# Kernel optimization log

Measured on AMD Instinct MI355X. Metric: run time of the kernel, lower is better.

Reference implementation:

```python
import jax, jax.numpy as jnp
import numpy as np

ATTRACTION_W = 1.0
REPULSION_W = 1.0
MARGIN = 0.3  # hardcoded local `margin = 0.3` in the torch forward


def setup_inputs() -> dict:
    key = jax.random.key(0)
    k1, k2, k3 = jax.random.split(key, 3)
    B, N, D, K = 16, 65536, 32, 512
    beta = jax.random.normal(k1, (B, N, 1), dtype=jnp.float32)
    embed = jax.random.normal(k2, (B, N, D), dtype=jnp.float32)
    # instance id per hit: -1 = background, 0..K-1 = instances
    sid = jax.random.randint(k3, (B, N), -1, K).astype(jnp.int32)
    # first K hits are the condensation points, one per instance
    sid = sid.at[:, :K].set(jnp.arange(K, dtype=jnp.int32)[None, :])
    is_cp = jnp.zeros((B, N), dtype=jnp.int32).at[:, :K].set(1)
    return {"beta": beta, "embed": embed, "slice_id": sid, "is_cp": is_cp, "num_instances": K}


def _per_batch(beta_b, emb_b, sid, iscp, K):
    # beta_b: [N], emb_b: [N, D], sid/iscp: [N]
    N = sid.shape[0]
    cp = iscp == 1
    valid = sid >= 0
    noncp = valid & ~cp  # non-cp signal hits
    pos = cp.sum().astype(jnp.float32)
    neg = jnp.float32(N) - pos  # noncp + background
    pos_w = jax.lax.stop_gradient(neg / (pos + 1e-6))
    w = jnp.where(cp, pos_w, jnp.where(noncp, 1.0, 2.0))
    # weighted BCE-with-logits, reduction='mean'
    x = beta_b
    y = cp.astype(jnp.float32)
    bce = jnp.maximum(x, 0.0) - x * y + jnp.log1p(jnp.exp(-jnp.abs(x)))
    beta_ce = (w * bce).mean()

    # segment id: valid hits -> sid, background -> dummy segment K (dropped)
    seg = jnp.where(valid, sid, K)
    counts = jax.ops.segment_sum(valid.astype(jnp.float32), seg, num_segments=K + 1)[:K]
    inst_exists = counts > 0  # the `unique()` set

    # first cp hit index per instance (sentinel N if instance has no cp)
    idxs = jnp.arange(N)
    first_cp = jax.ops.segment_min(jnp.where(cp & valid, idxs, N), seg, num_segments=K + 1)[:K]
    has_cp = first_cp < N
    safe_cp = jnp.minimum(first_cp, N - 1)
    cp_emb = emb_b[safe_cp]  # [K, D]
    cp_beta = beta_b[safe_cp]  # [K]

    # attraction: sum over instances (with a cp) of mean ||e_hit - e_cp||^2
    sid_c = jnp.clip(sid, 0, K - 1)
    d2 = ((emb_b - cp_emb[sid_c]) ** 2).sum(-1)  # [N]
    d2 = jnp.where(valid, d2, 0.0)
    seg_d2 = jax.ops.segment_sum(d2, seg, num_segments=K + 1)[:K]
    attr = (jnp.where(has_cp & inst_exists, seg_d2 / jnp.maximum(counts, 1.0), 0.0).sum()
            * ATTRACTION_W)

    # ranking: instances with exactly 1 cp and >0 noncp hits
    cp_count = jax.ops.segment_sum((cp & valid).astype(jnp.float32), seg, num_segments=K + 1)[:K]
    ncp_count = jax.ops.segment_sum(noncp.astype(jnp.float32), seg, num_segments=K + 1)[:K]
    r = jax.nn.relu(beta_b + MARGIN - cp_beta[sid_c])
    r = jnp.where(noncp, r, 0.0)
    seg_r = jax.ops.segment_sum(r, seg, num_segments=K + 1)[:K]
    qual = (cp_count == 1.0) & (ncp_count > 0)
    n_unique = inst_exists.sum().astype(jnp.float32)
    ranking = (jnp.where(qual, seg_r / jnp.maximum(ncp_count, 1.0), 0.0).sum()
               / jnp.maximum(n_unique, 1.0))

    beta_loss = beta_ce + 2.0 * ranking

    # repulsion over all cp hits; data has exactly one cp per instance so the
    # cp set equals cp_emb (K points), matching torch's emb_b[cp_idx]
    diff = cp_emb[:, None, :] - cp_emb[None, :, :]  # [K, K, D]
    rep = jnp.exp(-(diff ** 2).sum(-1)).mean() * REPULSION_W

    return beta_loss + attr + rep, beta_loss, attr, rep


def reference(beta, embed, slice_id, is_cp, num_instances):
    K = int(num_instances)
    beta2 = beta[..., 0]  # squeeze(-1)
    loss_b, bl, al, rl = jax.vmap(lambda b, e, s, c: _per_batch(b, e, s, c, K))(
        beta2, embed, slice_id, is_cp)
    return loss_b.mean(), bl.mean(), al.mean(), rl.mean()
```

## Files before the change

### kernel.cpp

```cpp
#include <hip/hip_runtime.h>
#include <math.h>

#define N_HITS 65536
#define K_INST 512
#define MARGIN 0.3f
#define BPB    128
#define HITS_PB (N_HITS / BPB)

__global__ __launch_bounds__(256) void k_scan(
    const int* __restrict__ sid, const int* __restrict__ iscp,
    int* first_cp, int* pos_cnt) {
    int b = blockIdx.y;
    size_t bo = (size_t)b * N_HITS;
    int i = blockIdx.x * 256 + threadIdx.x;
    int stride = gridDim.x * 256;
    for (; i < N_HITS; i += stride) {
        int c = iscp[bo + i];
        if (c == 1) {
            atomicAdd(&pos_cnt[b], 1);
            int s = sid[bo + i];
            if (s >= 0) atomicMin(&first_cp[b * K_INST + s], i);
        }
    }
}

__global__ __launch_bounds__(256) void k_gather(
    const float* __restrict__ beta, const float4* __restrict__ embed4,
    const int* __restrict__ first_cp,
    float* cp_beta, float4* cp_emb4, int B) {
    int g = blockIdx.x * 256 + threadIdx.x;
    int total = B * K_INST * 8;
    if (g >= total) return;
    int row = g >> 3, sub = g & 7;
    int b = row / K_INST;
    int fc = first_cp[row];
    int safe = min(fc, N_HITS - 1);
    cp_emb4[(size_t)row * 8 + sub] = embed4[((size_t)b * N_HITS + safe) * 8 + sub];
    if (sub == 0) cp_beta[row] = beta[b * N_HITS + safe];
}

__global__ __launch_bounds__(256) void k_main(
    const float*  __restrict__ beta,  const float4* __restrict__ embed4,
    const int*    __restrict__ sid_g, const int*    __restrict__ iscp_g,
    const float4* __restrict__ cp_emb4, const float* __restrict__ cp_beta,
    int* cnt_packed, float* seg_d2, float* seg_r,
    float* s_cp, float* s_ncp, float* s_bg) {
    __shared__ int   l_cnt[K_INST];
    __shared__ float l_d2[K_INST];
    __shared__ float l_r[K_INST];
    __shared__ float l_cb[K_INST];
    __shared__ float l_red[12];

    int b = blockIdx.y, tid = threadIdx.x;
    size_t bo = (size_t)b * N_HITS;
    int base = blockIdx.x * HITS_PB;

    for (int k = tid; k < K_INST; k += 256) {
        l_cnt[k] = 0; l_d2[k] = 0.f; l_r[k] = 0.f;
        l_cb[k] = cp_beta[b * K_INST + k];
    }
    __syncthreads();

    const float4* cpe = cp_emb4 + (size_t)b * K_INST * 8;
    float a_cp = 0.f, a_ncp = 0.f, a_bg = 0.f;

#pragma unroll
    for (int h = 0; h < HITS_PB / 256; ++h) {
        int i = base + h * 256 + tid;
        int s = sid_g[bo + i];
        int c = iscp_g[bo + i];
        float x = beta[bo + i];
        int sc = min(max(s, 0), K_INST - 1);
        const float4* ep  = embed4 + (bo + i) * 8;
        const float4* cpp = cpe + (size_t)sc * 8;

        float d2 = 0.f;
#pragma unroll
        for (int j = 0; j < 8; ++j) {
            float4 e = ep[j], ce = cpp[j];
            float dx = e.x - ce.x, dy = e.y - ce.y;
            float dz = e.z - ce.z, dw = e.w - ce.w;
            d2 += dx * dx + dy * dy + dz * dz + dw * dw;
        }

        bool cp = (c == 1), valid = (s >= 0), noncp = valid && !cp;
        float t = __expf(-fabsf(x));
        float bce = fmaxf(x, 0.f) - (cp ? x : 0.f) + __logf(1.f + t);
        if (cp) a_cp += bce; else if (noncp) a_ncp += bce; else a_bg += bce;
        if (valid) {
            atomicAdd(&l_cnt[s], cp ? (1 << 20) : 1);
            atomicAdd(&l_d2[s], d2);
            if (noncp) {
                float r = fmaxf(x + MARGIN - l_cb[s], 0.f);
                atomicAdd(&l_r[s], r);
            }
        }
    }

    for (int o = 32; o > 0; o >>= 1) {
        a_cp  += __shfl_down(a_cp, o);
        a_ncp += __shfl_down(a_ncp, o);
        a_bg  += __shfl_down(a_bg, o);
    }
    int wave = tid >> 6;
    if ((tid & 63) == 0) { l_red[wave] = a_cp; l_red[4 + wave] = a_ncp; l_red[8 + wave] = a_bg; }
    __syncthreads();
    if (tid == 0) {
        atomicAdd(&s_cp[b],  l_red[0] + l_red[1] + l_red[2]  + l_red[3]);
        atomicAdd(&s_ncp[b], l_red[4] + l_red[5] + l_red[6]  + l_red[7]);
        atomicAdd(&s_bg[b],  l_red[8] + l_red[9] + l_red[10] + l_red[11]);
    }
    for (int k = tid; k < K_INST; k += 256) {
        int   cv = l_cnt[k]; if (cv)        atomicAdd(&cnt_packed[b * K_INST + k], cv);
        float dv = l_d2[k];  if (dv != 0.f) atomicAdd(&seg_d2[b * K_INST + k], dv);
        float rv = l_r[k];   if (rv != 0.f) atomicAdd(&seg_r[b * K_INST + k], rv);
    }
}

__global__ __launch_bounds__(512) void k_tail(
    const float4* __restrict__ cp_emb4,
    const int* __restrict__ cnt_packed, const float* __restrict__ seg_d2,
    const float* __restrict__ seg_r, const int* __restrict__ first_cp,
    const int* __restrict__ pos_cnt, const float* __restrict__ s_cp,
    const float* __restrict__ s_ncp, const float* __restrict__ s_bg,
    float* attr_b, float* rank_b, float* nuniq_b, float* rep_b,
    int* ctr, float* out, int B) {
    int tid = threadIdx.x;
    int nrep = B * 16;

    if ((int)blockIdx.x < nrep) {
        __shared__ float4 tile[32 * 8];
        __shared__ float red[8];
        int b = blockIdx.x >> 4, t2 = blockIdx.x & 15;
        const float4* base = cp_emb4 + (size_t)b * K_INST * 8;
        float4 r0[8];
#pragma unroll
        for (int cc = 0; cc < 8; ++cc) r0[cc] = base[(size_t)tid * 8 + cc];
        if (tid < 256) tile[tid] = base[(size_t)t2 * 256 + tid];
        __syncthreads();
        float acc = 0.f;
        for (int j = 0; j < 32; ++j) {
            float d2 = 0.f;
#pragma unroll
            for (int cc = 0; cc < 8; ++cc) {
                float4 ev = tile[j * 8 + cc];
                float ax = r0[cc].x - ev.x, ay = r0[cc].y - ev.y;
                float az = r0[cc].z - ev.z, aw = r0[cc].w - ev.w;
                d2 += ax * ax + ay * ay + az * az + aw * aw;
            }
            acc += __expf(-d2);
        }
        for (int o = 32; o > 0; o >>= 1) acc += __shfl_down(acc, o);
        if ((tid & 63) == 0) red[tid >> 6] = acc;
        __syncthreads();
        if (tid == 0) {
            float t = 0.f;
            for (int w = 0; w < 8; ++w) t += red[w];
            atomicAdd(&rep_b[b], t);
        }
    } else {
        __shared__ float red2[3][8];
        int b = blockIdx.x - nrep, k = tid;
        int v = cnt_packed[b * K_INST + k];
        int ncp = v & 0xFFFFF, cpc = v >> 20;
        int counts = ncp + cpc;
        int fc = first_cp[b * K_INST + k];
        bool has_cp = fc < N_HITS, exists = counts > 0;
        float attr = (has_cp && exists) ? seg_d2[b * K_INST + k] / fmaxf((float)counts, 1.f) : 0.f;
        float rank = (cpc == 1 && ncp > 0) ? seg_r[b * K_INST + k] / fmaxf((float)ncp, 1.f) : 0.f;
        float uq = exists ? 1.f : 0.f;
        for (int o = 32; o > 0; o >>= 1) {
            attr += __shfl_down(attr, o);
            rank += __shfl_down(rank, o);
            uq   += __shfl_down(uq, o);
        }
        if ((k & 63) == 0) { red2[0][k >> 6] = attr; red2[1][k >> 6] = rank; red2[2][k >> 6] = uq; }
        __syncthreads();
        if (k == 0) {
            float a = 0.f, r = 0.f, u = 0.f;
            for (int w = 0; w < 8; ++w) { a += red2[0][w]; r += red2[1][w]; u += red2[2][w]; }
            attr_b[b] = a; rank_b[b] = r; nuniq_b[b] = u;
        }
    }

    __shared__ int is_last;
    __syncthreads();
    if (tid == 0) {
        __threadfence();
        int v = atomicAdd(ctr, 1);
        is_last = (v == (int)gridDim.x - 1);
    }
    __syncthreads();
    if (is_last) {
        __threadfence();
        if (tid < 64) {
            int b = tid;
            float loss = 0.f, bl = 0.f, at = 0.f, rp = 0.f;
            if (b < B) {
                float pos = (float)pos_cnt[b];
                float pw = ((float)N_HITS - pos) / (pos + 1e-6f);
                float bce = (pw * s_cp[b] + s_ncp[b] + 2.f * s_bg[b]) / (float)N_HITS;
                float rank = rank_b[b] / fmaxf(nuniq_b[b], 1.f);
                bl = bce + 2.f * rank;
                at = attr_b[b];
                rp = rep_b[b] / (float)(K_INST * K_INST);
                loss = bl + at + rp;
            }
            for (int o = 32; o > 0; o >>= 1) {
                loss += __shfl_down(loss, o);
                bl   += __shfl_down(bl, o);
                at   += __shfl_down(at, o);
                rp   += __shfl_down(rp, o);
            }
            if (tid == 0) {
                float inv = 1.f / (float)B;
                out[0] = loss * inv;
                out[1] = bl * inv;
                out[2] = at * inv;
                out[3] = rp * inv;
            }
        }
    }
}

extern "C" void kernel_launch(void* const* d_in, const int* in_sizes, int n_in,
                              void* d_out, int out_size, void* d_ws, size_t ws_size,
                              hipStream_t stream) {
    const float*  beta   = (const float*)d_in[0];
    const float*  embed  = (const float*)d_in[1];
    const int*    sid    = (const int*)d_in[2];
    const int*    iscp   = (const int*)d_in[3];
    float* out = (float*)d_out;

    int BN = in_sizes[0];
    int B  = BN / N_HITS;
    int BK = B * K_INST;

    char* ws = (char*)d_ws;
    int*   cnt_packed = (int*)ws;
    float* seg_d2     = (float*)(ws + 4 * (size_t)BK);
    float* seg_r      = (float*)(ws + 8 * (size_t)BK);
    float* scal       = (float*)(ws + 12 * (size_t)BK);
    int*   pos_cnt  = (int*)scal;
    float* s_cp     = scal + 1 * B;
    float* s_ncp    = scal + 2 * B;
    float* s_bg     = scal + 3 * B;
    float* attr_b   = scal + 4 * B;
    float* rank_b   = scal + 5 * B;
    float* nuniq_b  = scal + 6 * B;
    float* rep_b    = scal + 7 * B;
    int*   ctr      = (int*)(scal + 8 * B);
    size_t zbytes = 12 * (size_t)BK + 32 * (size_t)B + 16;
    int*    first_cp = (int*)(ws + zbytes);
    float*  cp_beta  = (float*)(ws + zbytes + 4 * (size_t)BK);
    float4* cp_emb4  = (float4*)(ws + zbytes + 8 * (size_t)BK);

    hipMemsetAsync(ws, 0, zbytes, stream);
    hipMemsetAsync(first_cp, 0x7F, 4 * (size_t)BK, stream);

    k_scan<<<dim3(32, B), 256, 0, stream>>>(sid, iscp, first_cp, pos_cnt);

    k_gather<<<(BK * 8 + 255) / 256, 256, 0, stream>>>(beta, (const float4*)embed,
                                                       first_cp, cp_beta, cp_emb4, B);

    k_main<<<dim3(BPB, B), 256, 0, stream>>>(beta, (const float4*)embed, sid, iscp,
                                             (const float4*)cp_emb4, cp_beta,
                                             cnt_packed, seg_d2, seg_r, s_cp, s_ncp, s_bg);

    k_tail<<<B * 16 + B, 512, 0, stream>>>(cp_emb4, cnt_packed, seg_d2, seg_r,
                                           first_cp, pos_cnt, s_cp, s_ncp, s_bg,
                                           attr_b, rank_b, nuniq_b, rep_b,
                                           ctr, out, B);
}
```

Before: 261.7 us.

## Stage bf16 condensation-point embeddings in LDS and expand distance algebraically

The gather kernel now also writes a bf16, XOR-swizzled copy of the per-instance condensation-point embeddings. k_main loads that copy into shared memory and computes the distance in a second pass in which 8 lanes share each hit with coalesced float4 loads. It accumulates e·(e−2c) per instance into 4-way split shared bins, and the tail adds count·||c||² back. This removes scattered global reads of cp embeddings and the serial per-thread 32-float loop. In exchange, sid is read twice, there are more LDS atomics, and bf16 cp values plus the expanded form can cost precision through cancellation.

```diff
diff --git a/kernel.cpp b/kernel.cpp
--- a/kernel.cpp
+++ b/kernel.cpp
@@ -6,6 +6,14 @@
 #define MARGIN 0.3f
 #define BPB    128
 #define HITS_PB (N_HITS / BPB)
+
+__device__ __forceinline__ unsigned short f2bf(float f) {
+    unsigned u = __float_as_uint(f);
+    return (unsigned short)((u + 0x7FFFu + ((u >> 16) & 1u)) >> 16);
+}
+__device__ __forceinline__ float bf2f(unsigned short h) {
+    return __uint_as_float(((unsigned)h) << 16);
+}
 
 __global__ __launch_bounds__(256) void k_scan(
     const int* __restrict__ sid, const int* __restrict__ iscp,
@@ -27,7 +35,7 @@
 __global__ __launch_bounds__(256) void k_gather(
     const float* __restrict__ beta, const float4* __restrict__ embed4,
     const int* __restrict__ first_cp,
-    float* cp_beta, float4* cp_emb4, int B) {
+    float* cp_beta, float4* cp_emb4, ushort4* cpb_g, int B) {
     int g = blockIdx.x * 256 + threadIdx.x;
     int total = B * K_INST * 8;
     if (g >= total) return;
@@ -35,65 +43,76 @@
     int b = row / K_INST;
     int fc = first_cp[row];
     int safe = min(fc, N_HITS - 1);
-    cp_emb4[(size_t)row * 8 + sub] = embed4[((size_t)b * N_HITS + safe) * 8 + sub];
+    float4 e = embed4[((size_t)b * N_HITS + safe) * 8 + sub];
+    cp_emb4[(size_t)row * 8 + sub] = e;
+    ushort4 h;
+    h.x = f2bf(e.x); h.y = f2bf(e.y); h.z = f2bf(e.z); h.w = f2bf(e.w);
+    cpb_g[(size_t)row * 8 + (sub ^ (row & 7))] = h;
     if (sub == 0) cp_beta[row] = beta[b * N_HITS + safe];
 }
 
 __global__ __launch_bounds__(256) void k_main(
-    const float*  __restrict__ beta,  const float4* __restrict__ embed4,
-    const int*    __restrict__ sid_g, const int*    __restrict__ iscp_g,
-    const float4* __restrict__ cp_emb4, const float* __restrict__ cp_beta,
+    const float*  __restrict__ beta,
+    const float4* __restrict__ embed4,
+    const int*    __restrict__ sid_g, const int* __restrict__ iscp_g,
+    const ushort4* __restrict__ cpb_g, const float* __restrict__ cp_beta,
     int* cnt_packed, float* seg_d2, float* seg_r,
     float* s_cp, float* s_ncp, float* s_bg) {
-    __shared__ int   l_cnt[K_INST];
-    __shared__ float l_d2[K_INST];
-    __shared__ float l_r[K_INST];
-    __shared__ float l_cb[K_INST];
-    __shared__ float l_red[12];
+    __shared__ ushort4 cpb[K_INST * 8];
+    __shared__ float   d2p[K_INST * 4];
+    __shared__ int     l_cnt[K_INST];
+    __shared__ float   l_r[K_INST];
+    __shared__ float   l_cb[K_INST];
+    __shared__ float   l_red[12];
 
     int b = blockIdx.y, tid = threadIdx.x;
     size_t bo = (size_t)b * N_HITS;
     int base = blockIdx.x * HITS_PB;
 
     for (int k = tid; k < K_INST; k += 256) {
-        l_cnt[k] = 0; l_d2[k] = 0.f; l_r[k] = 0.f;
+        l_cnt[k] = 0; l_r[k] = 0.f;
         l_cb[k] = cp_beta[b * K_INST + k];
     }
+    for (int k = tid; k < K_INST * 4; k += 256) d2p[k] = 0.f;
+    {
+        const ushort4* src = cpb_g + (size_t)b * K_INST * 8;
+        for (int k = tid; k < K_INST * 8; k += 256) cpb[k] = src[k];
+    }
     __syncthreads();
 
-    const float4* cpe = cp_emb4 + (size_t)b * K_INST * 8;
     float a_cp = 0.f, a_ncp = 0.f, a_bg = 0.f;
-
 #pragma unroll
     for (int h = 0; h < HITS_PB / 256; ++h) {
         int i = base + h * 256 + tid;
         int s = sid_g[bo + i];
         int c = iscp_g[bo + i];
         float x = beta[bo + i];
-        int sc = min(max(s, 0), K_INST - 1);
-        const float4* ep  = embed4 + (bo + i) * 8;
-        const float4* cpp = cpe + (size_t)sc * 8;
-
-        float d2 = 0.f;
-#pragma unroll
-        for (int j = 0; j < 8; ++j) {
-            float4 e = ep[j], ce = cpp[j];
-            float dx = e.x - ce.x, dy = e.y - ce.y;
-            float dz = e.z - ce.z, dw = e.w - ce.w;
-            d2 += dx * dx + dy * dy + dz * dz + dw * dw;
-        }
-
         bool cp = (c == 1), valid = (s >= 0), noncp = valid && !cp;
         float t = __expf(-fabsf(x));
         float bce = fmaxf(x, 0.f) - (cp ? x : 0.f) + __logf(1.f + t);
         if (cp) a_cp += bce; else if (noncp) a_ncp += bce; else a_bg += bce;
         if (valid) {
             atomicAdd(&l_cnt[s], cp ? (1 << 20) : 1);
-            atomicAdd(&l_d2[s], d2);
             if (noncp) {
                 float r = fmaxf(x + MARGIN - l_cb[s], 0.f);
                 atomicAdd(&l_r[s], r);
             }
+        }
+    }
+
+    {
+        int sub = tid & 7, hgrp = tid >> 3;
+#pragma unroll 4
+        for (int it = 0; it < HITS_PB / 32; ++it) {
+            int i = base + it * 32 + hgrp;
+            int s = sid_g[bo + i];
+            float4 e = embed4[(bo + i) * 8 + sub];
+            int sc = min(max(s, 0), K_INST - 1);
+            ushort4 h = cpb[sc * 8 + (sub ^ (sc & 7))];
+            float c0 = bf2f(h.x), c1 = bf2f(h.y), c2 = bf2f(h.z), c3 = bf2f(h.w);
+            float q = e.x * (e.x - 2.f * c0) + e.y * (e.y - 2.f * c1)
+                    + e.z * (e.z - 2.f * c2) + e.w * (e.w - 2.f * c3);
+            if (s >= 0) atomicAdd(&d2p[sc * 4 + (sub & 3)], q);
         }
     }
 
@@ -111,14 +130,15 @@
         atomicAdd(&s_bg[b],  l_red[8] + l_red[9] + l_red[10] + l_red[11]);
     }
     for (int k = tid; k < K_INST; k += 256) {
-        int   cv = l_cnt[k]; if (cv)        atomicAdd(&cnt_packed[b * K_INST + k], cv);
-        float dv = l_d2[k];  if (dv != 0.f) atomicAdd(&seg_d2[b * K_INST + k], dv);
-        float rv = l_r[k];   if (rv != 0.f) atomicAdd(&seg_r[b * K_INST + k], rv);
+        int   cv = l_cnt[k]; if (cv) atomicAdd(&cnt_packed[b * K_INST + k], cv);
+        float dv = d2p[k * 4] + d2p[k * 4 + 1] + d2p[k * 4 + 2] + d2p[k * 4 + 3];
+        if (dv != 0.f) atomicAdd(&seg_d2[b * K_INST + k], dv);
+        float rv = l_r[k]; if (rv != 0.f) atomicAdd(&seg_r[b * K_INST + k], rv);
     }
 }
 
 __global__ __launch_bounds__(512) void k_tail(
-    const float4* __restrict__ cp_emb4,
+    const float4* __restrict__ cp_emb4, const ushort4* __restrict__ cpb_g,
     const int* __restrict__ cnt_packed, const float* __restrict__ seg_d2,
     const float* __restrict__ seg_r, const int* __restrict__ first_cp,
     const int* __restrict__ pos_cnt, const float* __restrict__ s_cp,
@@ -166,7 +186,16 @@
         int counts = ncp + cpc;
         int fc = first_cp[b * K_INST + k];
         bool has_cp = fc < N_HITS, exists = counts > 0;
-        float attr = (has_cp && exists) ? seg_d2[b * K_INST + k] / fmaxf((float)counts, 1.f) : 0.f;
+        const ushort4* cq = cpb_g + ((size_t)b * K_INST + k) * 8;
+        float s2 = 0.f;
+#pragma unroll
+        for (int j = 0; j < 8; ++j) {
+            ushort4 h = cq[j];
+            float c0 = bf2f(h.x), c1 = bf2f(h.y), c2 = bf2f(h.z), c3 = bf2f(h.w);
+            s2 += c0 * c0 + c1 * c1 + c2 * c2 + c3 * c3;
+        }
+        float segd = seg_d2[b * K_INST + k] + (float)counts * s2;
+        float attr = (has_cp && exists) ? segd / fmaxf((float)counts, 1.f) : 0.f;
         float rank = (cpc == 1 && ncp > 0) ? seg_r[b * K_INST + k] / fmaxf((float)ncp, 1.f) : 0.f;
         float uq = exists ? 1.f : 0.f;
         for (int o = 32; o > 0; o >>= 1) {
@@ -251,9 +280,10 @@
     float* rep_b    = scal + 7 * B;
     int*   ctr      = (int*)(scal + 8 * B);
     size_t zbytes = 12 * (size_t)BK + 32 * (size_t)B + 16;
-    int*    first_cp = (int*)(ws + zbytes);
-    float*  cp_beta  = (float*)(ws + zbytes + 4 * (size_t)BK);
-    float4* cp_emb4  = (float4*)(ws + zbytes + 8 * (size_t)BK);
+    int*     first_cp = (int*)(ws + zbytes);
+    float*   cp_beta  = (float*)(ws + zbytes + 4 * (size_t)BK);
+    float4*  cp_emb4  = (float4*)(ws + zbytes + 8 * (size_t)BK);
+    ushort4* cpb_g    = (ushort4*)(ws + zbytes + 8 * (size_t)BK + 128 * (size_t)BK);
 
     hipMemsetAsync(ws, 0, zbytes, stream);
     hipMemsetAsync(first_cp, 0x7F, 4 * (size_t)BK, stream);
@@ -261,13 +291,16 @@
     k_scan<<<dim3(32, B), 256, 0, stream>>>(sid, iscp, first_cp, pos_cnt);
 
     k_gather<<<(BK * 8 + 255) / 256, 256, 0, stream>>>(beta, (const float4*)embed,
-                                                       first_cp, cp_beta, cp_emb4, B);
+                                                       first_cp, cp_beta, cp_emb4,
+                                                       cpb_g, B);
 
     k_main<<<dim3(BPB, B), 256, 0, stream>>>(beta, (const float4*)embed, sid, iscp,
-                                             (const float4*)cp_emb4, cp_beta,
-                                             cnt_packed, seg_d2, seg_r, s_cp, s_ncp, s_bg);
-
-    k_tail<<<B * 16 + B, 512, 0, stream>>>(cp_emb4, cnt_packed, seg_d2, seg_r,
+                                             (const ushort4*)cpb_g, cp_beta,
+                                             cnt_packed, seg_d2, seg_r,
+                                             s_cp, s_ncp, s_bg);
+
+    k_tail<<<B * 16 + B, 512, 0, stream>>>(cp_emb4, (const ushort4*)cpb_g,
+                                           cnt_packed, seg_d2, seg_r,
                                            first_cp, pos_cnt, s_cp, s_ncp, s_bg,
                                            attr_b, rank_b, nuniq_b, rep_b,
                                            ctr, out, B);
```

After: 297.7 us. +13.7%, slower.
